# Kernel optimization log

Measured on AMD Instinct MI355X. Metric: run time of the kernel, lower is better.

Reference implementation:

```python
import jax, jax.numpy as jnp
import numpy as np

VOCAB, EMB, HID, OUT = 50257, 256, 512, 2
SEQ, BATCH = 512, 64


def setup_inputs() -> dict:
    key = jax.random.key(0)
    ks = jax.random.split(key, 8)
    s_ih = 1.0 / np.sqrt(HID)
    return {
        "text": jax.random.randint(ks[0], (SEQ, BATCH), 0, VOCAB, dtype=jnp.int64)
            if jax.config.jax_enable_x64 else jax.random.randint(ks[0], (SEQ, BATCH), 0, VOCAB, dtype=jnp.int32),
        "emb_table": jax.random.normal(ks[1], (VOCAB, EMB), dtype=jnp.float32),
        "W_ih": jax.random.uniform(ks[2], (HID, EMB), jnp.float32, -s_ih, s_ih),
        "W_hh": jax.random.uniform(ks[3], (HID, HID), jnp.float32, -s_ih, s_ih),
        "b_ih": jax.random.uniform(ks[4], (HID,), jnp.float32, -s_ih, s_ih),
        "b_hh": jax.random.uniform(ks[5], (HID,), jnp.float32, -s_ih, s_ih),
        "W_fc": jax.random.uniform(ks[6], (OUT, HID), jnp.float32, -s_ih, s_ih),
        "b_fc": jax.random.uniform(ks[7], (OUT,), jnp.float32, -s_ih, s_ih),
    }


def reference(text, emb_table, W_ih, W_hh, b_ih, b_hh, W_fc, b_fc):
    # embedded: [seq, batch, emb]
    embedded = emb_table[text]
    h0 = jnp.zeros((text.shape[1], HID), dtype=emb_table.dtype)

    def step(h, x_t):
        # torch.nn.RNNCell (tanh): h' = tanh(x W_ih^T + b_ih + h W_hh^T + b_hh)
        h_new = jnp.tanh(x_t @ W_ih.T + b_ih + h @ W_hh.T + b_hh)
        return h_new, None

    h_final, _ = jax.lax.scan(step, h0, embedded)
    return h_final @ W_fc.T + b_fc
```

## Files before the change

### kernel.cpp

```cpp
#include <hip/hip_runtime.h>
#include <hip/hip_fp16.h>

#define SEQ   512
#define BATCH 64
#define EMB   256
#define HID   512

#define CR 192
#define CL 64
#define WLROW 68

typedef _Float16 half2v __attribute__((ext_vector_type(2)));
typedef _Float16 half8v __attribute__((ext_vector_type(8)));

__device__ __forceinline__ float dot2acc(half2v a, half2v b, float c) {
#if defined(__has_builtin)
#if __has_builtin(__builtin_amdgcn_fdot2)
  return __builtin_amdgcn_fdot2(a, b, c, false);
#else
  return fmaf((float)a[0], (float)b[0], fmaf((float)a[1], (float)b[1], c));
#endif
#else
  return fmaf((float)a[0], (float)b[0], fmaf((float)a[1], (float)b[1], c));
#endif
}

__device__ __forceinline__ float fast_tanh(float x) {
  x = fminf(fmaxf(x, -15.f), 15.f);
  float e = __expf(2.f * x);
  return (e - 1.f) / (e + 1.f);
}

__global__ __launch_bounds__(512, 2) void proj_kernel(
    const int* __restrict__ text, const float* __restrict__ emb,
    const float* __restrict__ Wih, const float* __restrict__ bih,
    const float* __restrict__ bhh, __half* __restrict__ X) {
  const int t = blockIdx.x;
  const int j = threadIdx.x;

  float acc[BATCH];
#pragma unroll
  for (int b = 0; b < BATCH; ++b) acc[b] = 0.f;

  for (int ec = 0; ec < EMB / 32; ++ec) {
    float w[32];
    const float4* wp = reinterpret_cast<const float4*>(Wih + (size_t)j * EMB + ec * 32);
#pragma unroll
    for (int q = 0; q < 8; ++q) {
      float4 v = wp[q];
      w[4 * q + 0] = v.x; w[4 * q + 1] = v.y; w[4 * q + 2] = v.z; w[4 * q + 3] = v.w;
    }
#pragma unroll
    for (int b = 0; b < BATCH; ++b) {
      int tok = __builtin_amdgcn_readfirstlane(text[t * BATCH + b]);
      const float* ar = emb + (size_t)tok * EMB + ec * 32;
#pragma unroll
      for (int e = 0; e < 32; ++e) acc[b] = fmaf(w[e], ar[e], acc[b]);
    }
  }

  const float bias = bih[j] + bhh[j];
#pragma unroll
  for (int b = 0; b < BATCH; ++b)
    X[((size_t)t * BATCH + b) * HID + j] = __float2half(acc[b] + bias);
}

__global__ __launch_bounds__(512, 2) void rnn_kernel(
    const __half* __restrict__ X, const float* __restrict__ Whh,
    const float* __restrict__ Wfc, const float* __restrict__ bfc,
    float* __restrict__ out) {
  __shared__ __align__(16) half2v Wl[HID * WLROW];
  __shared__ __align__(16) half2v h2[2][HID / 2];
  __shared__ float red[16];

  const int j = threadIdx.x;
  const int b = blockIdx.x;

  const float* wr = Whh + (size_t)j * HID;

  half2v w[CR];
#pragma unroll
  for (int c = 0; c < CR; ++c) {
    float2 v = reinterpret_cast<const float2*>(wr)[c];
    half2v h; h[0] = (_Float16)v.x; h[1] = (_Float16)v.y;
    w[c] = h;
  }
#pragma unroll
  for (int c = 0; c < CL; ++c) {
    float2 v = reinterpret_cast<const float2*>(wr)[CR + c];
    half2v h; h[0] = (_Float16)v.x; h[1] = (_Float16)v.y;
    Wl[j * WLROW + c] = h;
  }
  if (j < HID / 2) {
    half2v z; z[0] = (_Float16)0.f; z[1] = (_Float16)0.f;
    h2[0][j] = z;
  }
  __syncthreads();

  const __half* Xp = X + (size_t)b * HID + j;
  float xv = __half2float(Xp[0]);
  float h = 0.f;
  int cur = 0;

  for (int t = 0; t < SEQ; ++t) {
    const int tn = (t < SEQ - 1) ? t + 1 : t;
    float xnext = __half2float(Xp[(size_t)tn * BATCH * HID]);

    const half8v* hp = reinterpret_cast<const half8v*>(&h2[cur][0]);
    const half8v* wl = reinterpret_cast<const half8v*>(&Wl[j * WLROW]);

    float a0 = 0.f, a1 = 0.f, a2 = 0.f, a3 = 0.f;
#pragma unroll
    for (int q = 0; q < CR / 4; ++q) {
      half8v hv = hp[q];
      half2v h0 = {hv[0], hv[1]}, h1 = {hv[2], hv[3]};
      half2v h2p = {hv[4], hv[5]}, h3 = {hv[6], hv[7]};
      a0 = dot2acc(w[4 * q + 0], h0, a0);
      a1 = dot2acc(w[4 * q + 1], h1, a1);
      a2 = dot2acc(w[4 * q + 2], h2p, a2);
      a3 = dot2acc(w[4 * q + 3], h3, a3);
    }
#pragma unroll
    for (int q = 0; q < CL / 4; ++q) {
      half8v hv = hp[CR / 4 + q];
      half8v wv = wl[q];
      half2v h0 = {hv[0], hv[1]}, h1 = {hv[2], hv[3]};
      half2v h2p = {hv[4], hv[5]}, h3 = {hv[6], hv[7]};
      half2v w0 = {wv[0], wv[1]}, w1 = {wv[2], wv[3]};
      half2v w2 = {wv[4], wv[5]}, w3 = {wv[6], wv[7]};
      a0 = dot2acc(w0, h0, a0);
      a1 = dot2acc(w1, h1, a1);
      a2 = dot2acc(w2, h2p, a2);
      a3 = dot2acc(w3, h3, a3);
    }

    float acc = ((a0 + a1) + (a2 + a3)) + xv;
    h = fast_tanh(acc);
    xv = xnext;

    reinterpret_cast<__half*>(&h2[cur ^ 1][0])[j] = __float2half(h);
    __syncthreads();
    cur ^= 1;
  }

  float c0 = Wfc[j] * h;
  float c1 = Wfc[HID + j] * h;
#pragma unroll
  for (int o = 32; o > 0; o >>= 1) {
    c0 += __shfl_down(c0, o, 64);
    c1 += __shfl_down(c1, o, 64);
  }
  const int wave = j >> 6;
  if ((j & 63) == 0) { red[wave] = c0; red[8 + wave] = c1; }
  __syncthreads();
  if (j == 0) {
    float s0 = 0.f, s1 = 0.f;
#pragma unroll
    for (int i = 0; i < 8; ++i) { s0 += red[i]; s1 += red[8 + i]; }
    out[b * 2 + 0] = s0 + bfc[0];
    out[b * 2 + 1] = s1 + bfc[1];
  }
}

extern "C" void kernel_launch(void* const* d_in, const int* in_sizes, int n_in,
                              void* d_out, int out_size, void* d_ws, size_t ws_size,
                              hipStream_t stream) {
  const int*   text = (const int*)d_in[0];
  const float* emb  = (const float*)d_in[1];
  const float* Wih  = (const float*)d_in[2];
  const float* Whh  = (const float*)d_in[3];
  const float* bih  = (const float*)d_in[4];
  const float* bhh  = (const float*)d_in[5];
  const float* Wfc  = (const float*)d_in[6];
  const float* bfc  = (const float*)d_in[7];
  float* outp = (float*)d_out;

  __half* X = (__half*)d_ws;

  proj_kernel<<<SEQ, 512, 0, stream>>>(text, emb, Wih, bih, bhh, X);
  rnn_kernel<<<BATCH, 512, 0, stream>>>(X, Whh, Wfc, bfc, outp);
}
```

Before: 1.233 ms.

## Stage gathered embeddings in LDS as fp16 and use dot2 in projection

The projection kernel now gathers the 64 embedding rows for its timestep into shared memory once, converted to fp16. The inner product then runs on packed fp16 dot2 instructions over LDS data and fp16-converted W_ih, instead of each thread issuing scalar global loads of the embedding rows. This is meant to cut redundant global/scalar memory traffic and halve the multiply-add count. It costs 32KB of LDS, an extra barrier and reduced input precision. The launch-bounds hints also change: the rnn kernel's waves-per-EU hint becomes an explicit attribute, and the projection kernel drops its min-blocks hint.

Result: faster. 996.6 us (-19.1%).

```diff
diff --git a/kernel.cpp b/kernel.cpp
--- a/kernel.cpp
+++ b/kernel.cpp
@@ -31,31 +31,63 @@
   return (e - 1.f) / (e + 1.f);
 }
 
-__global__ __launch_bounds__(512, 2) void proj_kernel(
+__global__ __launch_bounds__(512) void proj_kernel(
     const int* __restrict__ text, const float* __restrict__ emb,
     const float* __restrict__ Wih, const float* __restrict__ bih,
     const float* __restrict__ bhh, __half* __restrict__ X) {
+  __shared__ __align__(16) __half se[BATCH][EMB];
+  __shared__ int stok[BATCH];
+
   const int t = blockIdx.x;
   const int j = threadIdx.x;
 
+  if (j < BATCH) stok[j] = text[t * BATCH + j];
+  __syncthreads();
+
+  {
+    const int r = j >> 3;
+    const int c0 = (j & 7) * 32;
+    const float4* src = reinterpret_cast<const float4*>(emb + (size_t)stok[r] * EMB + c0);
+    half2v* rowp = reinterpret_cast<half2v*>(&se[r][0]);
+#pragma unroll
+    for (int q = 0; q < 8; ++q) {
+      float4 v = src[q];
+      half2v p0; p0[0] = (_Float16)v.x; p0[1] = (_Float16)v.y;
+      half2v p1; p1[0] = (_Float16)v.z; p1[1] = (_Float16)v.w;
+      rowp[c0 / 2 + 2 * q + 0] = p0;
+      rowp[c0 / 2 + 2 * q + 1] = p1;
+    }
+  }
+  __syncthreads();
+
   float acc[BATCH];
 #pragma unroll
   for (int b = 0; b < BATCH; ++b) acc[b] = 0.f;
 
   for (int ec = 0; ec < EMB / 32; ++ec) {
-    float w[32];
+    half2v wh[16];
     const float4* wp = reinterpret_cast<const float4*>(Wih + (size_t)j * EMB + ec * 32);
 #pragma unroll
     for (int q = 0; q < 8; ++q) {
       float4 v = wp[q];
-      w[4 * q + 0] = v.x; w[4 * q + 1] = v.y; w[4 * q + 2] = v.z; w[4 * q + 3] = v.w;
+      wh[2 * q + 0][0] = (_Float16)v.x; wh[2 * q + 0][1] = (_Float16)v.y;
+      wh[2 * q + 1][0] = (_Float16)v.z; wh[2 * q + 1][1] = (_Float16)v.w;
     }
 #pragma unroll
     for (int b = 0; b < BATCH; ++b) {
-      int tok = __builtin_amdgcn_readfirstlane(text[t * BATCH + b]);
-      const float* ar = emb + (size_t)tok * EMB + ec * 32;
-#pragma unroll
-      for (int e = 0; e < 32; ++e) acc[b] = fmaf(w[e], ar[e], acc[b]);
+      const half8v* ep = reinterpret_cast<const half8v*>(&se[b][ec * 32]);
+      float a = acc[b];
+#pragma unroll
+      for (int r = 0; r < 4; ++r) {
+        half8v ev = ep[r];
+        half2v e0 = {ev[0], ev[1]}, e1 = {ev[2], ev[3]};
+        half2v e2 = {ev[4], ev[5]}, e3 = {ev[6], ev[7]};
+        a = dot2acc(wh[4 * r + 0], e0, a);
+        a = dot2acc(wh[4 * r + 1], e1, a);
+        a = dot2acc(wh[4 * r + 2], e2, a);
+        a = dot2acc(wh[4 * r + 3], e3, a);
+      }
+      acc[b] = a;
     }
   }
 
@@ -65,7 +97,9 @@
     X[((size_t)t * BATCH + b) * HID + j] = __float2half(acc[b] + bias);
 }
 
-__global__ __launch_bounds__(512, 2) void rnn_kernel(
+__global__ __launch_bounds__(512)
+__attribute__((amdgpu_waves_per_eu(2, 2)))
+void rnn_kernel(
     const __half* __restrict__ X, const float* __restrict__ Whh,
     const float* __restrict__ Wfc, const float* __restrict__ bfc,
     float* __restrict__ out) {
```
